# Optimization experiments

Hardware: AMD Instinct MI355X
Metric: run time of the kernel (lower is better)

Reference implementation:

```python
import jax, jax.numpy as jnp
import numpy as np

B, T, HOR, N = 32, 12, 12, 883
D = 10      # embed_dim == time_dim
HID = 64    # rnn_units
OUT = 1     # output_dim
K = 2       # cheb_k: supports [I, A]


def _pdg2(x, e1, e2, E, Wp, bp):
    # x:[B,N,Ci]  e1,e2:[B,N,D]  E:[N,D]  Wp:[D,K,Ci,Co]  bp:[D,Co]
    nv1 = jnp.tanh(E[None] * e1)                      # [B,N,D]
    nv2 = jnp.tanh(E[None] * e2)
    A = jax.nn.softmax(jax.nn.relu(jnp.einsum('bnd,bmd->bnm', nv1, nv2)), axis=-1)
    xg = jnp.stack([x, jnp.einsum('bnm,bmc->bnc', A, x)], axis=2)   # [B,N,K,Ci]
    W = jnp.einsum('bnd,dkio->bnkio', nv1, Wp)        # node/time-adaptive weights
    b = jnp.einsum('bnd,do->bno', nv1, bp)
    return jnp.einsum('bnki,bnkio->bno', xg, W) + b


def _cell(x, h, e1, e2, E, gW, gb, uW, ub):
    xs = jnp.concatenate([x, h], axis=-1)
    zr = jax.nn.sigmoid(_pdg2(xs, e1, e2, E, gW, gb))
    z, r = jnp.split(zr, 2, axis=-1)
    cand = jnp.concatenate([x, z * h], axis=-1)
    hc = jnp.tanh(_pdg2(cand, e1, e2, E, uW, ub))
    return r * h + (1.0 - r) * hc


def setup_inputs() -> dict:
    key = jax.random.key(0)
    ks = jax.random.split(key, 20)
    s = 0.1
    inp = {
        'src_vals': jax.random.normal(ks[0], (B, T, N, 1), jnp.float32),
        'node_emb': s * jax.random.normal(ks[1], (N, D), jnp.float32),
        'tid_emb1': s * jax.random.normal(ks[2], (288, D), jnp.float32),
        'tid_emb2': s * jax.random.normal(ks[3], (288, D), jnp.float32),
        'diw_emb1': s * jax.random.normal(ks[4], (7, D), jnp.float32),
        'diw_emb2': s * jax.random.normal(ks[5], (7, D), jnp.float32),
        'enc_gate_W': s * jax.random.normal(ks[6], (D, K, 1 + HID, 2 * HID), jnp.float32),
        'enc_gate_b': s * jax.random.normal(ks[7], (D, 2 * HID), jnp.float32),
        'enc_upd_W': s * jax.random.normal(ks[8], (D, K, 1 + HID, HID), jnp.float32),
        'enc_upd_b': s * jax.random.normal(ks[9], (D, HID), jnp.float32),
        'dec_gate_W': s * jax.random.normal(ks[10], (D, K, OUT + HID, 2 * HID), jnp.float32),
        'dec_gate_b': s * jax.random.normal(ks[11], (D, 2 * HID), jnp.float32),
        'dec_upd_W': s * jax.random.normal(ks[12], (D, K, OUT + HID, HID), jnp.float32),
        'dec_upd_b': s * jax.random.normal(ks[13], (D, HID), jnp.float32),
        'proj_W': s * jax.random.normal(ks[14], (OUT, HID), jnp.float32),
        'proj_b': jnp.zeros((OUT,), jnp.float32),
        'src_tid': jax.random.randint(ks[15], (B, T, N), 0, 288, jnp.int32),
        'src_diw': jax.random.randint(ks[16], (B, T, N), 0, 7, jnp.int32),
        'tgt_tid': jax.random.randint(ks[17], (B, HOR, N), 0, 288, jnp.int32),
        'tgt_diw': jax.random.randint(ks[18], (B, HOR, N), 0, 7, jnp.int32),
    }
    return inp


def reference(src_vals, node_emb, tid_emb1, tid_emb2, diw_emb1, diw_emb2,
              enc_gate_W, enc_gate_b, enc_upd_W, enc_upd_b,
              dec_gate_W, dec_gate_b, dec_upd_W, dec_upd_b,
              proj_W, proj_b, src_tid, src_diw, tgt_tid, tgt_diw):
    tm = lambda a: jnp.swapaxes(a, 0, 1)   # batch-major -> time-major
    # periodic embeddings (use_week=True -> elementwise product)
    e1_en = tid_emb1[src_tid] * diw_emb1[src_diw]   # [B,T,N,D]
    e2_en = tid_emb2[src_tid] * diw_emb2[src_diw]
    e1_de = tid_emb1[tgt_tid] * diw_emb1[tgt_diw]   # [B,HOR,N,D]
    e2_de = tid_emb2[tgt_tid] * diw_emb2[tgt_diw]

    h0 = jnp.zeros((src_vals.shape[0], node_emb.shape[0], HID), src_vals.dtype)

    def enc_step(h, inp):
        x, e1, e2 = inp
        h = _cell(x, h, e1, e2, node_emb, enc_gate_W, enc_gate_b, enc_upd_W, enc_upd_b)
        return h, None

    h, _ = jax.lax.scan(enc_step, h0, (tm(src_vals), tm(e1_en), tm(e2_en)))

    go0 = jnp.zeros((src_vals.shape[0], node_emb.shape[0], OUT), src_vals.dtype)

    def dec_step(carry, inp):
        h, go = carry
        e1, e2 = inp
        h = _cell(go, h, e1, e2, node_emb, dec_gate_W, dec_gate_b, dec_upd_W, dec_upd_b)
        go = h @ proj_W.T + proj_b
        return (h, go), go

    _, outs = jax.lax.scan(dec_step, (h, go0), (tm(e1_de), tm(e2_de)))
    return jnp.swapaxes(outs, 0, 1)   # [B,HOR,N,OUT]
```

## Files before the change

kernel.cpp:

```cpp
#include <hip/hip_runtime.h>

#define BB 32
#define TSRC 12
#define HORZ 12
#define NN 883
#define DD 10
#define HH 64
#define BN (BB*NN)
#define BNP 28288
#define KF 5
#define NT 14

typedef __attribute__((ext_vector_type(8))) short short8;
typedef __attribute__((ext_vector_type(4))) float f32x4;

static __device__ __forceinline__ float sigmf(float x) { return 1.f/(1.f + __expf(-x)); }
static __device__ __forceinline__ float tanh_fast(float x) {
  float e = __expf(2.f*x);
  return (e - 1.f) / (e + 1.f);
}
static __device__ __forceinline__ unsigned int bf_hi(float f) {
  unsigned int u = __float_as_uint(f);
  return (u + 0x7fffu + ((u >> 16) & 1u)) >> 16;
}
static __device__ __forceinline__ float bf_f(unsigned int h) {
  return __uint_as_float(h << 16);
}
static __device__ __forceinline__ void lds_load16(const void* g, void* l) {
  __builtin_amdgcn_global_load_lds(
      (const __attribute__((address_space(1))) void*)g,
      (__attribute__((address_space(3))) void*)l, 16, 0, 0);
}

static __device__ __forceinline__ void xs_store(unsigned short* chunk, int c, int mm2, float v) {
  int p0 = (c*128 + (mm2 ^ ((c & 7) << 4))) >> 1;
  unsigned int hi = bf_hi(v);
  chunk[p0] = (unsigned short)hi;
  chunk[p0 + 4096] = (unsigned short)bf_hi(v - bf_f(hi));
}

__global__ __launch_bounds__(256) void prep_kernel(
    const float* __restrict__ tidE1, const float* __restrict__ tidE2,
    const float* __restrict__ diwE1, const float* __restrict__ diwE2,
    const float* __restrict__ nodeE,
    const int* __restrict__ tididx, const int* __restrict__ diwidx,
    const float* __restrict__ xsrc, int xmode, int t, int tlen,
    float* __restrict__ nv1T, float* __restrict__ nv2T,
    unsigned short* __restrict__ XsH, unsigned short* __restrict__ XsZ)
{
  int i = blockIdx.x*256 + threadIdx.x;
  if (i >= BN) return;
  int b = i / NN, n = i - b*NN;
  int gi = (b*tlen + t)*NN + n;
  int ti = tididx[gi]*DD, di = diwidx[gi]*DD;
  int nE = n*DD;
#pragma unroll
  for (int d = 0; d < DD; ++d) {
    float E = nodeE[nE+d];
    nv1T[d*BNP+i] = tanh_fast(E * (tidE1[ti+d] * diwE1[di+d]));
    nv2T[d*BNP+i] = tanh_fast(E * (tidE2[ti+d] * diwE2[di+d]));
  }
  float xv = (xmode == 0) ? xsrc[gi] : xsrc[i];
  size_t cb = ((size_t)(b*NT + (n >> 6)))*8192;
  int mm = n & 63;
  unsigned int hi = bf_hi(xv);
  unsigned short los = (unsigned short)bf_hi(xv - bf_f(hi));
  XsH[cb + mm] = (unsigned short)hi; XsH[cb + 4096 + mm] = los;
  XsZ[cb + mm] = (unsigned short)hi; XsZ[cb + 4096 + mm] = los;
}

__global__ __launch_bounds__(256) void wsplit_kernel(
    const float* __restrict__ W, const float* __restrict__ bias,
    int NO, unsigned short* __restrict__ Wf)
{
  int i = blockIdx.x*256 + threadIdx.x;
  int total = DD*2*KF*4*NO*8;
  if (i >= total) return;
  int j = i & 7; int r = i >> 3;
  int o = r % NO; r /= NO;
  int quad = r & 3; r >>= 2;
  int kf = r % KF; r /= KF;
  int hl = r & 1; int d = r >> 1;
  int kk = kf*32 + quad*8 + j;
  float v = 0.f;
  if (kk <= 64)       v = W[(size_t)(d*130 + kk)*NO + o];
  else if (kk == 65)  v = bias[d*NO + o];
  else if (kk <= 130) v = W[(size_t)(d*130 + kk - 1)*NO + o];
  unsigned int hi = bf_hi(v);
  Wf[i] = (hl == 0) ? (unsigned short)hi : (unsigned short)bf_hi(v - bf_f(hi));
}

__global__ __launch_bounds__(256,3) void attn_kernel(
    const float* __restrict__ nv1T, const float* __restrict__ nv2T,
    const unsigned short* __restrict__ Xs,
    const float* __restrict__ hsrc,
    float* __restrict__ axT)
{
  __shared__ float nv1s[DD][64];
  __shared__ float nv2s[2][DD][64];
  __shared__ float xcolb[2][64];
  __shared__ alignas(16) unsigned short XT[8192];
  __shared__ alignas(16) unsigned short PT[2][64][72];
  __shared__ float linv[64];
  int b = blockIdx.y;
  int r0 = blockIdx.x*64;
  int tid = threadIdx.x;
  int rg = tid >> 4, cg = tid & 15;
  int base = b*NN;
  int lane = tid & 63, lm = lane & 15, quad = lane >> 4;
  int w = tid >> 6, mp = w >> 1, np = w & 1;
  const unsigned short* XsB = Xs + (size_t)b*NT*8192;

  for (int idx = tid; idx < DD*64; idx += 256) {
    int d = idx >> 6, r = idx & 63;
    nv1s[d][r] = (r0 + r < NN) ? nv1T[d*BNP + base + r0 + r] : 0.f;
  }

  int4 xt[4];
  float nvr[3]; float xcr;
  {
    const int4* s0 = (const int4*)XsB;
#pragma unroll
    for (int i = 0; i < 4; ++i) xt[i] = s0[w*64 + lane + i*256];
#pragma unroll
    for (int i = 0; i < 3; ++i) {
      int idx = tid + i*256; float v = 0.f;
      if (idx < DD*64) { int d = idx>>6, m = idx&63; v = (m < NN) ? nv2T[d*BNP + base + m] : 0.f; }
      nvr[i] = v;
    }
    xcr = (tid < 64 && tid < NN) ? hsrc[(size_t)63*BNP + base + tid] : 0.f;
#pragma unroll
    for (int i = 0; i < 4; ++i)
      *(int4*)((char*)XT + w*1024 + lane*16 + i*4096) = xt[i];
#pragma unroll
    for (int i = 0; i < 3; ++i) {
      int idx = tid + i*256;
      if (idx < DD*64) (&nv2s[0][0][0])[idx] = nvr[i];
    }
    if (tid < 64) xcolb[0][tid] = xcr;
  }
  __syncthreads();

  f32x4 accv[2][2] = {};
  float acclp[4] = {}, acc5p[4] = {};

  for (int tI = 0; tI < NT; ++tI) {
    int cur = tI & 1, nxt = cur ^ 1;
    int m0 = tI*64, m0n = m0 + 64;
    bool hasn = tI < NT-1;
    if (hasn) {
      const int4* src = (const int4*)(XsB + (size_t)(tI+1)*8192);
#pragma unroll
      for (int i = 0; i < 4; ++i) xt[i] = src[w*64 + lane + i*256];
#pragma unroll
      for (int i = 0; i < 3; ++i) {
        int idx = tid + i*256; float v = 0.f;
        if (idx < DD*64) { int d = idx>>6, m = idx&63; v = (m0n + m < NN) ? nv2T[d*BNP + base + m0n + m] : 0.f; }
        nvr[i] = v;
      }
      xcr = (tid < 64 && m0n + tid < NN) ? hsrc[(size_t)63*BNP + base + m0n + tid] : 0.f;
    }
    float s[4][4] = {};
#pragma unroll
    for (int d = 0; d < DD; ++d) {
      float4 a4 = *(const float4*)&nv1s[d][rg*4];
      float4 c4 = *(const float4*)&nv2s[cur][d][cg*4];
      const float* ap = (const float*)&a4;
      const float* cp = (const float*)&c4;
#pragma unroll
      for (int j = 0; j < 4; ++j)
#pragma unroll
        for (int jj = 0; jj < 4; ++jj)
          s[j][jj] += ap[j]*cp[jj];
    }
    int mvlim = NN - m0;
    float ev[4][4];
#pragma unroll
    for (int jj = 0; jj < 4; ++jj) {
      int m = cg*4 + jj;
      float xm = xcolb[cur][m];
      bool okm = m < mvlim;
#pragma unroll
      for (int j = 0; j < 4; ++j) {
        float e = okm ? __expf(fmaxf(s[j][jj], 0.f)) : 0.f;
        ev[j][jj] = e;
        acclp[j] += e;
        acc5p[j] = fmaf(e, xm, acc5p[j]);
      }
    }
    {
      unsigned int* P1 = (unsigned int*)&PT[0][0][0];
      unsigned int* P2 = (unsigned int*)&PT[1][0][0];
#pragma unroll
      for (int j = 0; j < 4; ++j) {
        int r = rg*4 + j;
        unsigned int h0 = bf_hi(ev[j][0]), h1 = bf_hi(ev[j][1]), h2 = bf_hi(ev[j][2]), h3 = bf_hi(ev[j][3]);
        unsigned int l0 = bf_hi(ev[j][0]-bf_f(h0)), l1 = bf_hi(ev[j][1]-bf_f(h1));
        unsigned int l2 = bf_hi(ev[j][2]-bf_f(h2)), l3 = bf_hi(ev[j][3]-bf_f(h3));
        int dw = r*36 + cg*2;
        P1[dw] = h0 | (h1 << 16); P1[dw+1] = h2 | (h3 << 16);
        P2[dw] = l0 | (l1 << 16); P2[dw+1] = l2 | (l3 << 16);
      }
    }
    __syncthreads();
    {
      short8 Aa[2][2], Ab[2][2], Ba[2][2], Bb[2][2];
#pragma unroll
      for (int mt = 0; mt < 2; ++mt) {
        int r = mp*32 + mt*16 + lm;
#pragma unroll
        for (int kf = 0; kf < 2; ++kf) {
          Aa[mt][kf] = *(const short8*)&PT[0][r][quad*8 + kf*32];
          Ab[mt][kf] = *(const short8*)&PT[1][r][quad*8 + kf*32];
        }
      }
#pragma unroll
      for (int ntl = 0; ntl < 2; ++ntl) {
        int c = np*32 + ntl*16 + lm;
        int swz = (c & 7) << 4;
        int cb0 = c*128 + quad*16;
#pragma unroll
        for (int kf = 0; kf < 2; ++kf) {
          int a = (cb0 + kf*64) ^ swz;
          Ba[ntl][kf] = *(const short8*)((const char*)XT + a);
          Bb[ntl][kf] = *(const short8*)((const char*)XT + a + 8192);
        }
      }
#pragma unroll
      for (int kf = 0; kf < 2; ++kf)
#pragma unroll
        for (int mt = 0; mt < 2; ++mt)
#pragma unroll
          for (int ntl = 0; ntl < 2; ++ntl) {
            accv[mt][ntl] = __builtin_amdgcn_mfma_f32_16x16x32_bf16(Aa[mt][kf], Ba[ntl][kf], accv[mt][ntl], 0,0,0);
            accv[mt][ntl] = __builtin_amdgcn_mfma_f32_16x16x32_bf16(Aa[mt][kf], Bb[ntl][kf], accv[mt][ntl], 0,0,0);
            accv[mt][ntl] = __builtin_amdgcn_mfma_f32_16x16x32_bf16(Ab[mt][kf], Ba[ntl][kf], accv[mt][ntl], 0,0,0);
          }
    }
    if (hasn) {
#pragma unroll
      for (int i = 0; i < 3; ++i) {
        int idx = tid + i*256;
        if (idx < DD*64) (&nv2s[nxt][0][0])[idx] = nvr[i];
      }
      if (tid < 64) xcolb[nxt][tid] = xcr;
    }
    __syncthreads();
    if (hasn) {
#pragma unroll
      for (int i = 0; i < 4; ++i)
        *(int4*)((char*)XT + w*1024 + lane*16 + i*4096) = xt[i];
    }
  }
#pragma unroll
  for (int off = 1; off <= 8; off <<= 1)
#pragma unroll
    for (int j = 0; j < 4; ++j) {
      acclp[j] += __shfl_xor(acclp[j], off, 64);
      acc5p[j] += __shfl_xor(acc5p[j], off, 64);
    }
  __syncthreads();
  if (cg == 0) {
#pragma unroll
    for (int j = 0; j < 4; ++j) {
      float li = 1.f / acclp[j];
      linv[rg*4 + j] = li;
      int r = r0 + rg*4 + j;
      if (r < NN) axT[(size_t)64*BNP + base + r] = acc5p[j]*li;
    }
  }
  __syncthreads();
  float* CT = (float*)&PT[0][0][0];
#pragma unroll
  for (int mt = 0; mt < 2; ++mt) {
    float4 lv = *(const float4*)&linv[mp*32 + mt*16 + quad*4];
    const float* lvp = (const float*)&lv;
#pragma unroll
    for (int ntl = 0; ntl < 2; ++ntl) {
      int c = np*32 + ntl*16 + lm;
#pragma unroll
      for (int r4 = 0; r4 < 4; ++r4)
        CT[(mp*32 + mt*16 + quad*4 + r4)*69 + c] = accv[mt][ntl][r4]*lvp[r4];
    }
  }
  __syncthreads();
  {
    int r = tid & 63, cb = tid >> 6;
    bool ok = (r0 + r) < NN;
    int gr = base + r0 + r;
#pragma unroll 4
    for (int i = 0; i < 16; ++i) {
      int c = cb*16 + i;
      if (ok) axT[(size_t)c*BNP + gr] = CT[r*69 + c];
    }
  }
}


__global__ __launch_bounds__(256,3) void gate_mfma(
    const float* __restrict__ xsrc, int xmode, int t, int tlen,
    const float* __restrict__ h,
    const float* __restrict__ axT,
    const float* __restrict__ nv1T,
    const unsigned short* __restrict__ Wf,
    float* __restrict__ zh, float* __restrict__ rbuf,
    unsigned short* __restrict__ XsZ)
{
  __shared__ alignas(16) unsigned char smem[46080];
  __shared__ float nvs[DD][64];
  unsigned short* XA = (unsigned short*)smem;
  unsigned int*  X1 = (unsigned int*)smem;
  int n0 = blockIdx.x*64, co0 = blockIdx.y*64;
  int tid = threadIdx.x;
  {
    int m = tid >> 2, ksub = tid & 3;
    int gm = n0 + m;
    float xv;
    if (xmode == 0) { int b = gm/NN; int n = gm - b*NN; xv = (gm < BN) ? xsrc[(b*tlen+t)*NN + n] : 0.f; }
    else xv = xsrc[gm];
#pragma unroll 4
    for (int i = 0; i < 20; ++i) {
      int kk = ksub*2 + 8*i;
      float v0, v1;
      if (kk == 0)        v0 = xv;
      else if (kk <= 64)  v0 = h[(size_t)(kk-1)*BNP + gm];
      else if (kk == 65)  v0 = 1.f;
      else if (kk <= 130) v0 = axT[(size_t)(kk-66)*BNP + gm];
      else v0 = 0.f;
      int k1 = kk + 1;
      if (k1 <= 64)       v1 = h[(size_t)(k1-1)*BNP + gm];
      else if (k1 == 65)  v1 = 1.f;
      else if (k1 <= 130) v1 = axT[(size_t)(k1-66)*BNP + gm];
      else v1 = 0.f;
      unsigned int h0 = bf_hi(v0), h1 = bf_hi(v1);
      unsigned int l0 = bf_hi(v0 - bf_f(h0)), l1 = bf_hi(v1 - bf_f(h1));
      int kf = kk >> 5, kkl = kk & 31;
      int dw = (kf*64 + m)*36 + (kkl >> 1);
      X1[dw] = h0 | (h1 << 16);
      X1[dw + 16] = l0 | (l1 << 16);
    }
  }
  for (int idx = tid; idx < DD*64; idx += 256)
    nvs[idx>>6][idx&63] = nv1T[(size_t)(idx>>6)*BNP + n0 + (idx&63)];
  __syncthreads();
  int w = tid >> 6, lane = tid & 63;
  int lm = lane & 15, quad = lane >> 4;
  int mp = w >> 1, np = w & 1;
  short8 A1[2][KF], A2[2][KF];
#pragma unroll
  for (int mt = 0; mt < 2; ++mt) {
    int mrow = mp*32 + mt*16 + lm;
#pragma unroll
    for (int kf = 0; kf < KF; ++kf) {
      A1[mt][kf] = *(const short8*)&XA[(kf*64 + mrow)*72 + quad*8];
      A2[mt][kf] = *(const short8*)&XA[(kf*64 + mrow)*72 + 32 + quad*8];
    }
  }
  __syncthreads();
  unsigned char* bufA = smem;
  unsigned char* bufB = smem + 20480;
  const int colb = np*32 + lm;
  {
    const unsigned short* src = Wf + ((size_t)(w*5)*128 + co0)*8 + lane*8;
#pragma unroll
    for (int i = 0; i < 5; ++i)
      lds_load16(src + (size_t)i*128*8, bufA + (w*5+i)*1024);
  }
  f32x4 accO[2][2] = {};
#pragma unroll 1
  for (int d = 0; d < DD; ++d) {
    f32x4 td[2][2] = {};
    __syncthreads();
    {
      const unsigned short* src = Wf + ((size_t)((d*2+1)*20 + w*5)*128 + co0)*8 + lane*8;
#pragma unroll
      for (int i = 0; i < 5; ++i)
        lds_load16(src + (size_t)i*128*8, bufB + (w*5+i)*1024);
    }
#pragma unroll
    for (int kf = 0; kf < KF; ++kf) {
      int cb = ((kf*4 + quad)*64 + colb)*16;
#pragma unroll
      for (int ntl = 0; ntl < 2; ++ntl) {
        short8 Bh = *(const short8*)(bufA + cb + ntl*256);
        td[0][ntl] = __builtin_amdgcn_mfma_f32_16x16x32_bf16(A1[0][kf], Bh, td[0][ntl], 0,0,0);
        td[0][ntl] = __builtin_amdgcn_mfma_f32_16x16x32_bf16(A2[0][kf], Bh, td[0][ntl], 0,0,0);
        td[1][ntl] = __builtin_amdgcn_mfma_f32_16x16x32_bf16(A1[1][kf], Bh, td[1][ntl], 0,0,0);
        td[1][ntl] = __builtin_amdgcn_mfma_f32_16x16x32_bf16(A2[1][kf], Bh, td[1][ntl], 0,0,0);
      }
    }
    __syncthreads();
    if (d < DD-1) {
      const unsigned short* src = Wf + ((size_t)((d+1)*2*20 + w*5)*128 + co0)*8 + lane*8;
#pragma unroll
      for (int i = 0; i < 5; ++i)
        lds_load16(src + (size_t)i*128*8, bufA + (w*5+i)*1024);
    }
#pragma unroll
    for (int kf = 0; kf < KF; ++kf) {
      int cb = ((kf*4 + quad)*64 + colb)*16;
#pragma unroll
      for (int ntl = 0; ntl < 2; ++ntl) {
        short8 Bl = *(const short8*)(bufB + cb + ntl*256);
        td[0][ntl] = __builtin_amdgcn_mfma_f32_16x16x32_bf16(A1[0][kf], Bl, td[0][ntl], 0,0,0);
        td[1][ntl] = __builtin_amdgcn_mfma_f32_16x16x32_bf16(A1[1][kf], Bl, td[1][ntl], 0,0,0);
      }
    }
#pragma unroll
    for (int mt = 0; mt < 2; ++mt) {
      float4 nv4 = *(const float4*)&nvs[d][mp*32 + mt*16 + quad*4];
      const float* nvp = (const float*)&nv4;
#pragma unroll
      for (int ntl = 0; ntl < 2; ++ntl)
#pragma unroll
        for (int r = 0; r < 4; ++r)
          accO[mt][ntl][r] += nvp[r] * td[mt][ntl][r];
    }
  }
  float* CT = (float*)smem;
  __syncthreads();
#pragma unroll
  for (int mt = 0; mt < 2; ++mt)
#pragma unroll
    for (int ntl = 0; ntl < 2; ++ntl)
#pragma unroll
      for (int r = 0; r < 4; ++r)
        CT[(mp*32 + mt*16 + quad*4 + r)*67 + np*32 + ntl*16 + lm] = accO[mt][ntl][r];
  __syncthreads();
  {
    int mm = tid & 63, og = tid >> 6;
    int gm = n0 + mm;
    if (co0 == 0) {
      bool okg = gm < BN;
      int bb = okg ? (gm / NN) : 0;
      int ml = gm - bb*NN;
      unsigned short* chk = XsZ + ((size_t)(bb*NT + (ml >> 6)))*8192;
      int mm2 = (ml & 63)*2;
      for (int j = 0; j < 16; ++j) {
        int o = og*16 + j;
        float z = sigmf(CT[mm*67 + o]);
        float zhv = z * h[(size_t)o*BNP + gm];
        zh[(size_t)o*BNP + gm] = zhv;
        if (okg && o < 63) xs_store(chk, o + 1, mm2, zhv);
      }
    } else {
      for (int j = 0; j < 16; ++j) {
        int o = og*16 + j;
        rbuf[(size_t)o*BNP + gm] = sigmf(CT[mm*67 + o]);
      }
    }
  }
}

__global__ __launch_bounds__(256,3) void upd_mfma(
    const float* __restrict__ xsrc, int xmode, int t, int tlen,
    const float* __restrict__ zh,
    const float* __restrict__ axT,
    const float* __restrict__ nv1T,
    const unsigned short* __restrict__ Wf,
    const float* __restrict__ rbuf, float* __restrict__ h,
    int dec, const float* __restrict__ pW, const float* __restrict__ pb,
    float* __restrict__ go, float* __restrict__ dout,
    unsigned short* __restrict__ XsH)
{
  __shared__ alignas(16) unsigned char smem[46080];
  __shared__ float nvs[DD][64];
  unsigned short* XA = (unsigned short*)smem;
  unsigned int*  X1 = (unsigned int*)smem;
  int n0 = blockIdx.x*64;
  int tid = threadIdx.x;
  {
    int m = tid >> 2, ksub = tid & 3;
    int gm = n0 + m;
    float xv;
    if (xmode == 0) { int b = gm/NN; int n = gm - b*NN; xv = (gm < BN) ? xsrc[(b*tlen+t)*NN + n] : 0.f; }
    else xv = xsrc[gm];
#pragma unroll 4
    for (int i = 0; i < 20; ++i) {
      int kk = ksub*2 + 8*i;
      float v0, v1;
      if (kk == 0)        v0 = xv;
      else if (kk <= 64)  v0 = zh[(size_t)(kk-1)*BNP + gm];
      else if (kk == 65)  v0 = 1.f;
      else if (kk <= 130) v0 = axT[(size_t)(kk-66)*BNP + gm];
      else v0 = 0.f;
      int k1 = kk + 1;
      if (k1 <= 64)       v1 = zh[(size_t)(k1-1)*BNP + gm];
      else if (k1 == 65)  v1 = 1.f;
      else if (k1 <= 130) v1 = axT[(size_t)(k1-66)*BNP + gm];
      else v1 = 0.f;
      unsigned int h0 = bf_hi(v0), h1 = bf_hi(v1);
      unsigned int l0 = bf_hi(v0 - bf_f(h0)), l1 = bf_hi(v1 - bf_f(h1));
      int kf = kk >> 5, kkl = kk & 31;
      int dw = (kf*64 + m)*36 + (kkl >> 1);
      X1[dw] = h0 | (h1 << 16);
      X1[dw + 16] = l0 | (l1 << 16);
    }
  }
  for (int idx = tid; idx < DD*64; idx += 256)
    nvs[idx>>6][idx&63] = nv1T[(size_t)(idx>>6)*BNP + n0 + (idx&63)];
  __syncthreads();
  int w = tid >> 6, lane = tid & 63;
  int lm = lane & 15, quad = lane >> 4;
  int mp = w >> 1, np = w & 1;
  short8 A1[2][KF], A2[2][KF];
#pragma unroll
  for (int mt = 0; mt < 2; ++mt) {
    int mrow = mp*32 + mt*16 + lm;
#pragma unroll
    for (int kf = 0; kf < KF; ++kf) {
      A1[mt][kf] = *(const short8*)&XA[(kf*64 + mrow)*72 + quad*8];
      A2[mt][kf] = *(const short8*)&XA[(kf*64 + mrow)*72 + 32 + quad*8];
    }
  }
  __syncthreads();
  unsigned char* bufA = smem;
  unsigned char* bufB = smem + 20480;
  const int colb = np*32 + lm;
  {
    const unsigned short* src = Wf + (size_t)(w*5)*64*8 + lane*8;
#pragma unroll
    for (int i = 0; i < 5; ++i)
      lds_load16(src + (size_t)i*64*8, bufA + (w*5+i)*1024);
  }
  f32x4 accO[2][2] = {};
#pragma unroll 1
  for (int d = 0; d < DD; ++d) {
    f32x4 td[2][2] = {};
    __syncthreads();
    {
      const unsigned short* src = Wf + (size_t)((d*2+1)*20 + w*5)*64*8 + lane*8;
#pragma unroll
      for (int i = 0; i < 5; ++i)
        lds_load16(src + (size_t)i*64*8, bufB + (w*5+i)*1024);
    }
#pragma unroll
    for (int kf = 0; kf < KF; ++kf) {
      int cb = ((kf*4 + quad)*64 + colb)*16;
#pragma unroll
      for (int ntl = 0; ntl < 2; ++ntl) {
        short8 Bh = *(const short8*)(bufA + cb + ntl*256);
        td[0][ntl] = __builtin_amdgcn_mfma_f32_16x16x32_bf16(A1[0][kf], Bh, td[0][ntl], 0,0,0);
        td[0][ntl] = __builtin_amdgcn_mfma_f32_16x16x32_bf16(A2[0][kf], Bh, td[0][ntl], 0,0,0);
        td[1][ntl] = __builtin_amdgcn_mfma_f32_16x16x32_bf16(A1[1][kf], Bh, td[1][ntl], 0,0,0);
        td[1][ntl] = __builtin_amdgcn_mfma_f32_16x16x32_bf16(A2[1][kf], Bh, td[1][ntl], 0,0,0);
      }
    }
    __syncthreads();
    if (d < DD-1) {
      const unsigned short* src = Wf + (size_t)((d+1)*2*20 + w*5)*64*8 + lane*8;
#pragma unroll
      for (int i = 0; i < 5; ++i)
        lds_load16(src + (size_t)i*64*8, bufA + (w*5+i)*1024);
    }
#pragma unroll
    for (int kf = 0; kf < KF; ++kf) {
      int cb = ((kf*4 + quad)*64 + colb)*16;
#pragma unroll
      for (int ntl = 0; ntl < 2; ++ntl) {
        short8 Bl = *(const short8*)(bufB + cb + ntl*256);
        td[0][ntl] = __builtin_amdgcn_mfma_f32_16x16x32_bf16(A1[0][kf], Bl, td[0][ntl], 0,0,0);
        td[1][ntl] = __builtin_amdgcn_mfma_f32_16x16x32_bf16(A1[1][kf], Bl, td[1][ntl], 0,0,0);
      }
    }
#pragma unroll
    for (int mt = 0; mt < 2; ++mt) {
      float4 nv4 = *(const float4*)&nvs[d][mp*32 + mt*16 + quad*4];
      const float* nvp = (const float*)&nv4;
#pragma unroll
      for (int ntl = 0; ntl < 2; ++ntl)
#pragma unroll
        for (int r = 0; r < 4; ++r)
          accO[mt][ntl][r] += nvp[r] * td[mt][ntl][r];
    }
  }
  float* CT = (float*)smem;
  __syncthreads();
#pragma unroll
  for (int mt = 0; mt < 2; ++mt)
#pragma unroll
    for (int ntl = 0; ntl < 2; ++ntl)
#pragma unroll
      for (int r = 0; r < 4; ++r)
        CT[(mp*32 + mt*16 + quad*4 + r)*67 + np*32 + ntl*16 + lm] = accO[mt][ntl][r];
  __syncthreads();
  {
    int mm = tid & 63, og = tid >> 6;
    int gm = n0 + mm;
    bool okg = gm < BN;
    int bb = okg ? (gm / NN) : 0;
    int ml = gm - bb*NN;
    unsigned short* chk = XsH + ((size_t)(bb*NT + (ml >> 6)))*8192;
    int mm2 = (ml & 63)*2;
    float pp = 0.f;
    for (int j = 0; j < 16; ++j) {
      int o = og*16 + j;
      float hc = tanhf(CT[mm*67 + o]);
      float r = rbuf[(size_t)o*BNP + gm];
      float hv = h[(size_t)o*BNP + gm];
      float hn = r*hv + (1.f - r)*hc;
      h[(size_t)o*BNP + gm] = hn;
      if (okg && o < 63) xs_store(chk, o + 1, mm2, hn);
      if (dec) pp = fmaf(hn, pW[o], pp);
    }
    if (dec) {
      float* PS = CT + 64*67;
      __syncthreads();
      PS[mm*4 + og] = pp;
      __syncthreads();
      if (tid < 64 && gm < BN) {
        float s = pb[0] + PS[tid*4] + PS[tid*4+1] + PS[tid*4+2] + PS[tid*4+3];
        go[gm] = s;
        int b = gm/NN, n = gm - b*NN;
        dout[(b*HORZ + t)*NN + n] = s;
      }
    }
  }
}

extern "C" void kernel_launch(void* const* d_in, const int* in_sizes, int n_in,
                              void* d_out, int out_size, void* d_ws, size_t ws_size,
                              hipStream_t stream) {
  (void)in_sizes; (void)n_in; (void)out_size; (void)ws_size;
  const float* src_vals = (const float*)d_in[0];
  const float* node_emb = (const float*)d_in[1];
  const float* tid1 = (const float*)d_in[2];
  const float* tid2 = (const float*)d_in[3];
  const float* diw1 = (const float*)d_in[4];
  const float* diw2 = (const float*)d_in[5];
  const float* egW = (const float*)d_in[6];
  const float* egb = (const float*)d_in[7];
  const float* euW = (const float*)d_in[8];
  const float* eub = (const float*)d_in[9];
  const float* dgW = (const float*)d_in[10];
  const float* dgb = (const float*)d_in[11];
  const float* duW = (const float*)d_in[12];
  const float* dub = (const float*)d_in[13];
  const float* pW  = (const float*)d_in[14];
  const float* pb  = (const float*)d_in[15];
  const int* stid = (const int*)d_in[16];
  const int* sdiw = (const int*)d_in[17];
  const int* ttid = (const int*)d_in[18];
  const int* tdiw = (const int*)d_in[19];
  float* out = (float*)d_out;

  float* wp = (float*)d_ws;
  float* hbuf = wp; wp += (size_t)64*BNP;
  float* zh   = wp; wp += (size_t)64*BNP;
  float* rbuf = wp; wp += (size_t)64*BNP;
  float* axT  = wp; wp += (size_t)65*BNP;
  float* nv1T = wp; wp += (size_t)DD*BNP;
  float* nv2T = wp; wp += (size_t)DD*BNP;
  float* go   = wp; wp += BN + 64;
  unsigned short* egS = (unsigned short*)wp; wp += 204800;
  unsigned short* dgS = (unsigned short*)wp; wp += 204800;
  unsigned short* euS = (unsigned short*)wp; wp += 102400;
  unsigned short* duS = (unsigned short*)wp; wp += 102400;
  unsigned short* XsH = (unsigned short*)wp; wp += 1835008;
  unsigned short* XsZ = (unsigned short*)wp; wp += 1835008;

  hipMemsetAsync(hbuf, 0, sizeof(float)*(size_t)64*BNP, stream);
  hipMemsetAsync(go, 0, sizeof(float)*(BN+64), stream);
  hipMemsetAsync(XsH, 0, (size_t)BB*NT*16384, stream);
  hipMemsetAsync(XsZ, 0, (size_t)BB*NT*16384, stream);

  wsplit_kernel<<<1600,256,0,stream>>>(egW, egb, 128, egS);
  wsplit_kernel<<<1600,256,0,stream>>>(dgW, dgb, 128, dgS);
  wsplit_kernel<<<800,256,0,stream>>>(euW, eub, 64, euS);
  wsplit_kernel<<<800,256,0,stream>>>(duW, dub, 64, duS);

  dim3 agrid(NT, BB);
  dim3 ggrid(442, 2);
  for (int t = 0; t < TSRC; ++t) {
    prep_kernel<<<111,256,0,stream>>>(tid1,tid2,diw1,diw2,node_emb,stid,sdiw,src_vals,0,t,TSRC,nv1T,nv2T,XsH,XsZ);
    attn_kernel<<<agrid,256,0,stream>>>(nv1T,nv2T,XsH,hbuf,axT);
    gate_mfma<<<ggrid,256,0,stream>>>(src_vals,0,t,TSRC,hbuf,axT,nv1T,egS,zh,rbuf,XsZ);
    attn_kernel<<<agrid,256,0,stream>>>(nv1T,nv2T,XsZ,zh,axT);
    upd_mfma<<<442,256,0,stream>>>(src_vals,0,t,TSRC,zh,axT,nv1T,euS,rbuf,hbuf,0,pW,pb,go,out,XsH);
  }
  for (int t = 0; t < HORZ; ++t) {
    prep_kernel<<<111,256,0,stream>>>(tid1,tid2,diw1,diw2,node_emb,ttid,tdiw,go,1,t,HORZ,nv1T,nv2T,XsH,XsZ);
    attn_kernel<<<agrid,256,0,stream>>>(nv1T,nv2T,XsH,hbuf,axT);
    gate_mfma<<<ggrid,256,0,stream>>>(go,1,t,HORZ,hbuf,axT,nv1T,dgS,zh,rbuf,XsZ);
    attn_kernel<<<agrid,256,0,stream>>>(nv1T,nv2T,XsZ,zh,axT);
    upd_mfma<<<442,256,0,stream>>>(go,1,t,HORZ,zh,axT,nv1T,duS,rbuf,hbuf,1,pW,pb,go,out,XsH);
  }
}
```

Baseline: 4.863 ms.

## Fuse graph attention with gate and update GEMMs into per-block kernels

Merges the attention kernel with the following gate and update MFMA kernels so that the aggregated A·x result is written straight into shared memory as bf16 hi/lo operands. It no longer goes through the global axT buffer. This removes the axT write and re-read and two launches per cell step. In exchange, each fused block now covers both gate output halves serially over a 14x32 grid rather than 442x2. That reduces parallelism and may leave the GPU underfilled during the GEMM phase.

```diff
diff --git a/kernel.cpp b/kernel.cpp
--- a/kernel.cpp
+++ b/kernel.cpp
@@ -90,20 +90,24 @@
   Wf[i] = (hl == 0) ? (unsigned short)hi : (unsigned short)bf_hi(v - bf_f(hi));
 }
 
-__global__ __launch_bounds__(256,3) void attn_kernel(
+
+__global__ __launch_bounds__(256,3) void attn_gate(
     const float* __restrict__ nv1T, const float* __restrict__ nv2T,
     const unsigned short* __restrict__ Xs,
     const float* __restrict__ hsrc,
-    float* __restrict__ axT)
+    const float* __restrict__ xsrc, int xmode, int t, int tlen,
+    const unsigned short* __restrict__ Wf,
+    float* __restrict__ zh, float* __restrict__ rbuf,
+    unsigned short* __restrict__ XsZ)
 {
   __shared__ float nv1s[DD][64];
-  __shared__ float nv2s[2][DD][64];
-  __shared__ float xcolb[2][64];
-  __shared__ alignas(16) unsigned short XT[8192];
-  __shared__ alignas(16) unsigned short PT[2][64][72];
   __shared__ float linv[64];
-  int b = blockIdx.y;
-  int r0 = blockIdx.x*64;
+  __shared__ alignas(16) unsigned char U[46080];
+  unsigned short* XT = (unsigned short*)U;
+  unsigned short* PT = (unsigned short*)(U + 16384);
+  float* nv2s = (float*)(U + 34816);
+  float* xcolb = (float*)(U + 39936);
+  int b = blockIdx.y, r0 = blockIdx.x*64;
   int tid = threadIdx.x;
   int rg = tid >> 4, cg = tid & 15;
   int base = b*NN;
@@ -135,9 +139,9 @@
 #pragma unroll
     for (int i = 0; i < 3; ++i) {
       int idx = tid + i*256;
-      if (idx < DD*64) (&nv2s[0][0][0])[idx] = nvr[i];
-    }
-    if (tid < 64) xcolb[0][tid] = xcr;
+      if (idx < DD*64) nv2s[idx] = nvr[i];
+    }
+    if (tid < 64) xcolb[tid] = xcr;
   }
   __syncthreads();
 
@@ -164,7 +168,7 @@
 #pragma unroll
     for (int d = 0; d < DD; ++d) {
       float4 a4 = *(const float4*)&nv1s[d][rg*4];
-      float4 c4 = *(const float4*)&nv2s[cur][d][cg*4];
+      float4 c4 = *(const float4*)&nv2s[cur*(DD*64) + d*64 + cg*4];
       const float* ap = (const float*)&a4;
       const float* cp = (const float*)&c4;
 #pragma unroll
@@ -178,7 +182,7 @@
 #pragma unroll
     for (int jj = 0; jj < 4; ++jj) {
       int m = cg*4 + jj;
-      float xm = xcolb[cur][m];
+      float xm = xcolb[cur*64 + m];
       bool okm = m < mvlim;
 #pragma unroll
       for (int j = 0; j < 4; ++j) {
@@ -189,8 +193,8 @@
       }
     }
     {
-      unsigned int* P1 = (unsigned int*)&PT[0][0][0];
-      unsigned int* P2 = (unsigned int*)&PT[1][0][0];
+      unsigned int* P1 = (unsigned int*)PT;
+      unsigned int* P2 = (unsigned int*)(PT + 64*72);
 #pragma unroll
       for (int j = 0; j < 4; ++j) {
         int r = rg*4 + j;
@@ -210,8 +214,8 @@
         int r = mp*32 + mt*16 + lm;
 #pragma unroll
         for (int kf = 0; kf < 2; ++kf) {
-          Aa[mt][kf] = *(const short8*)&PT[0][r][quad*8 + kf*32];
-          Ab[mt][kf] = *(const short8*)&PT[1][r][quad*8 + kf*32];
+          Aa[mt][kf] = *(const short8*)&PT[r*72 + quad*8 + kf*32];
+          Ab[mt][kf] = *(const short8*)&PT[64*72 + r*72 + quad*8 + kf*32];
         }
       }
 #pragma unroll
@@ -241,15 +245,31 @@
 #pragma unroll
       for (int i = 0; i < 3; ++i) {
         int idx = tid + i*256;
-        if (idx < DD*64) (&nv2s[nxt][0][0])[idx] = nvr[i];
-      }
-      if (tid < 64) xcolb[nxt][tid] = xcr;
+        if (idx < DD*64) nv2s[nxt*(DD*64) + idx] = nvr[i];
+      }
+      if (tid < 64) xcolb[nxt*64 + tid] = xcr;
     }
     __syncthreads();
     if (hasn) {
 #pragma unroll
       for (int i = 0; i < 4; ++i)
         *(int4*)((char*)XT + w*1024 + lane*16 + i*4096) = xt[i];
+    }
+  }
+  int mrow_x = tid >> 2, ksub = tid & 3;
+  int gmx = base + r0 + mrow_x;
+  float hv0[9], hv1[9];
+  {
+    bool nok = (r0 + mrow_x) < NN;
+    float xv;
+    if (xmode == 0) xv = nok ? xsrc[(b*tlen+t)*NN + r0 + mrow_x] : 0.f;
+    else xv = xsrc[gmx];
+#pragma unroll
+    for (int i = 0; i < 9; ++i) {
+      int kk = ksub*2 + 8*i;
+      if (kk > 64) { hv0[i] = 0.f; hv1[i] = 0.f; continue; }
+      hv0[i] = (kk == 0) ? xv : hsrc[(size_t)(kk-1)*BNP + gmx];
+      hv1[i] = (kk == 64) ? 1.f : hsrc[(size_t)kk*BNP + gmx];
     }
   }
 #pragma unroll
@@ -260,92 +280,61 @@
       acc5p[j] += __shfl_xor(acc5p[j], off, 64);
     }
   __syncthreads();
+  {
+    unsigned int* Z = (unsigned int*)(U + 36864);
+    for (int idx = tid; idx < 2304; idx += 256) Z[idx] = 0;
+  }
+  __syncthreads();
+  unsigned short* XA = (unsigned short*)U;
   if (cg == 0) {
 #pragma unroll
     for (int j = 0; j < 4; ++j) {
       float li = 1.f / acclp[j];
-      linv[rg*4 + j] = li;
-      int r = r0 + rg*4 + j;
-      if (r < NN) axT[(size_t)64*BNP + base + r] = acc5p[j]*li;
-    }
-  }
-  __syncthreads();
-  float* CT = (float*)&PT[0][0][0];
+      int r = rg*4 + j;
+      linv[r] = li;
+      float v = acc5p[j]*li;
+      unsigned int hi = bf_hi(v);
+      XA[(4*64 + r)*72 + 2] = (unsigned short)hi;
+      XA[(4*64 + r)*72 + 32 + 2] = (unsigned short)bf_hi(v - bf_f(hi));
+    }
+  }
+  __syncthreads();
 #pragma unroll
   for (int mt = 0; mt < 2; ++mt) {
-    float4 lv = *(const float4*)&linv[mp*32 + mt*16 + quad*4];
+    int rbase = mp*32 + mt*16 + quad*4;
+    float4 lv = *(const float4*)&linv[rbase];
     const float* lvp = (const float*)&lv;
 #pragma unroll
     for (int ntl = 0; ntl < 2; ++ntl) {
       int c = np*32 + ntl*16 + lm;
-#pragma unroll
-      for (int r4 = 0; r4 < 4; ++r4)
-        CT[(mp*32 + mt*16 + quad*4 + r4)*69 + c] = accv[mt][ntl][r4]*lvp[r4];
-    }
-  }
-  __syncthreads();
-  {
-    int r = tid & 63, cb = tid >> 6;
-    bool ok = (r0 + r) < NN;
-    int gr = base + r0 + r;
-#pragma unroll 4
-    for (int i = 0; i < 16; ++i) {
-      int c = cb*16 + i;
-      if (ok) axT[(size_t)c*BNP + gr] = CT[r*69 + c];
-    }
-  }
-}
-
-
-__global__ __launch_bounds__(256,3) void gate_mfma(
-    const float* __restrict__ xsrc, int xmode, int t, int tlen,
-    const float* __restrict__ h,
-    const float* __restrict__ axT,
-    const float* __restrict__ nv1T,
-    const unsigned short* __restrict__ Wf,
-    float* __restrict__ zh, float* __restrict__ rbuf,
-    unsigned short* __restrict__ XsZ)
-{
-  __shared__ alignas(16) unsigned char smem[46080];
-  __shared__ float nvs[DD][64];
-  unsigned short* XA = (unsigned short*)smem;
-  unsigned int*  X1 = (unsigned int*)smem;
-  int n0 = blockIdx.x*64, co0 = blockIdx.y*64;
-  int tid = threadIdx.x;
-  {
-    int m = tid >> 2, ksub = tid & 3;
-    int gm = n0 + m;
-    float xv;
-    if (xmode == 0) { int b = gm/NN; int n = gm - b*NN; xv = (gm < BN) ? xsrc[(b*tlen+t)*NN + n] : 0.f; }
-    else xv = xsrc[gm];
-#pragma unroll 4
-    for (int i = 0; i < 20; ++i) {
+      int kk = 66 + c;
+      int kf = kk >> 5, kkl = kk & 31;
+#pragma unroll
+      for (int r4 = 0; r4 < 4; ++r4) {
+        float v = accv[mt][ntl][r4] * lvp[r4];
+        unsigned int hi = bf_hi(v);
+        int p = (kf*64 + rbase + r4)*72 + kkl;
+        XA[p] = (unsigned short)hi;
+        XA[p + 32] = (unsigned short)bf_hi(v - bf_f(hi));
+      }
+    }
+  }
+  {
+    unsigned int* X1 = (unsigned int*)U;
+#pragma unroll
+    for (int i = 0; i < 9; ++i) {
       int kk = ksub*2 + 8*i;
-      float v0, v1;
-      if (kk == 0)        v0 = xv;
-      else if (kk <= 64)  v0 = h[(size_t)(kk-1)*BNP + gm];
-      else if (kk == 65)  v0 = 1.f;
-      else if (kk <= 130) v0 = axT[(size_t)(kk-66)*BNP + gm];
-      else v0 = 0.f;
-      int k1 = kk + 1;
-      if (k1 <= 64)       v1 = h[(size_t)(k1-1)*BNP + gm];
-      else if (k1 == 65)  v1 = 1.f;
-      else if (k1 <= 130) v1 = axT[(size_t)(k1-66)*BNP + gm];
-      else v1 = 0.f;
+      if (kk > 64) continue;
+      float v0 = hv0[i], v1 = hv1[i];
       unsigned int h0 = bf_hi(v0), h1 = bf_hi(v1);
       unsigned int l0 = bf_hi(v0 - bf_f(h0)), l1 = bf_hi(v1 - bf_f(h1));
       int kf = kk >> 5, kkl = kk & 31;
-      int dw = (kf*64 + m)*36 + (kkl >> 1);
+      int dw = (kf*64 + mrow_x)*36 + (kkl >> 1);
       X1[dw] = h0 | (h1 << 16);
       X1[dw + 16] = l0 | (l1 << 16);
     }
   }
-  for (int idx = tid; idx < DD*64; idx += 256)
-    nvs[idx>>6][idx&63] = nv1T[(size_t)(idx>>6)*BNP + n0 + (idx&63)];
-  __syncthreads();
-  int w = tid >> 6, lane = tid & 63;
-  int lm = lane & 15, quad = lane >> 4;
-  int mp = w >> 1, np = w & 1;
+  __syncthreads();
   short8 A1[2][KF], A2[2][KF];
 #pragma unroll
   for (int mt = 0; mt < 2; ++mt) {
@@ -357,152 +346,354 @@
     }
   }
   __syncthreads();
-  unsigned char* bufA = smem;
-  unsigned char* bufB = smem + 20480;
+  unsigned char* bufA = U;
+  unsigned char* bufB = U + 20480;
   const int colb = np*32 + lm;
-  {
-    const unsigned short* src = Wf + ((size_t)(w*5)*128 + co0)*8 + lane*8;
-#pragma unroll
-    for (int i = 0; i < 5; ++i)
-      lds_load16(src + (size_t)i*128*8, bufA + (w*5+i)*1024);
-  }
-  f32x4 accO[2][2] = {};
 #pragma unroll 1
-  for (int d = 0; d < DD; ++d) {
-    f32x4 td[2][2] = {};
+  for (int co = 0; co < 2; ++co) {
+    int co0 = co*64;
+    {
+      const unsigned short* src = Wf + ((size_t)(w*5)*128 + co0)*8 + lane*8;
+#pragma unroll
+      for (int i = 0; i < 5; ++i)
+        lds_load16(src + (size_t)i*128*8, bufA + (w*5+i)*1024);
+    }
+    f32x4 accO[2][2] = {};
+#pragma unroll 1
+    for (int d = 0; d < DD; ++d) {
+      f32x4 td[2][2] = {};
+      __syncthreads();
+      {
+        const unsigned short* src = Wf + ((size_t)((d*2+1)*20 + w*5)*128 + co0)*8 + lane*8;
+#pragma unroll
+        for (int i = 0; i < 5; ++i)
+          lds_load16(src + (size_t)i*128*8, bufB + (w*5+i)*1024);
+      }
+#pragma unroll
+      for (int kf = 0; kf < KF; ++kf) {
+        int cb = ((kf*4 + quad)*64 + colb)*16;
+#pragma unroll
+        for (int ntl = 0; ntl < 2; ++ntl) {
+          short8 Bh = *(const short8*)(bufA + cb + ntl*256);
+          td[0][ntl] = __builtin_amdgcn_mfma_f32_16x16x32_bf16(A1[0][kf], Bh, td[0][ntl], 0,0,0);
+          td[0][ntl] = __builtin_amdgcn_mfma_f32_16x16x32_bf16(A2[0][kf], Bh, td[0][ntl], 0,0,0);
+          td[1][ntl] = __builtin_amdgcn_mfma_f32_16x16x32_bf16(A1[1][kf], Bh, td[1][ntl], 0,0,0);
+          td[1][ntl] = __builtin_amdgcn_mfma_f32_16x16x32_bf16(A2[1][kf], Bh, td[1][ntl], 0,0,0);
+        }
+      }
+      __syncthreads();
+      if (d < DD-1) {
+        const unsigned short* src = Wf + ((size_t)((d+1)*2*20 + w*5)*128 + co0)*8 + lane*8;
+#pragma unroll
+        for (int i = 0; i < 5; ++i)
+          lds_load16(src + (size_t)i*128*8, bufA + (w*5+i)*1024);
+      }
+#pragma unroll
+      for (int kf = 0; kf < KF; ++kf) {
+        int cb = ((kf*4 + quad)*64 + colb)*16;
+#pragma unroll
+        for (int ntl = 0; ntl < 2; ++ntl) {
+          short8 Bl = *(const short8*)(bufB + cb + ntl*256);
+          td[0][ntl] = __builtin_amdgcn_mfma_f32_16x16x32_bf16(A1[0][kf], Bl, td[0][ntl], 0,0,0);
+          td[1][ntl] = __builtin_amdgcn_mfma_f32_16x16x32_bf16(A1[1][kf], Bl, td[1][ntl], 0,0,0);
+        }
+      }
+#pragma unroll
+      for (int mt = 0; mt < 2; ++mt) {
+        float4 nv4 = *(const float4*)&nv1s[d][mp*32 + mt*16 + quad*4];
+        const float* nvp = (const float*)&nv4;
+#pragma unroll
+        for (int ntl = 0; ntl < 2; ++ntl)
+#pragma unroll
+          for (int r = 0; r < 4; ++r)
+            accO[mt][ntl][r] += nvp[r] * td[mt][ntl][r];
+      }
+    }
+    float* CT = (float*)U;
+    __syncthreads();
+#pragma unroll
+    for (int mt = 0; mt < 2; ++mt)
+#pragma unroll
+      for (int ntl = 0; ntl < 2; ++ntl)
+#pragma unroll
+        for (int r = 0; r < 4; ++r)
+          CT[(mp*32 + mt*16 + quad*4 + r)*67 + np*32 + ntl*16 + lm] = accO[mt][ntl][r];
     __syncthreads();
     {
-      const unsigned short* src = Wf + ((size_t)((d*2+1)*20 + w*5)*128 + co0)*8 + lane*8;
-#pragma unroll
-      for (int i = 0; i < 5; ++i)
-        lds_load16(src + (size_t)i*128*8, bufB + (w*5+i)*1024);
-    }
-#pragma unroll
-    for (int kf = 0; kf < KF; ++kf) {
-      int cb = ((kf*4 + quad)*64 + colb)*16;
-#pragma unroll
-      for (int ntl = 0; ntl < 2; ++ntl) {
-        short8 Bh = *(const short8*)(bufA + cb + ntl*256);
-        td[0][ntl] = __builtin_amdgcn_mfma_f32_16x16x32_bf16(A1[0][kf], Bh, td[0][ntl], 0,0,0);
-        td[0][ntl] = __builtin_amdgcn_mfma_f32_16x16x32_bf16(A2[0][kf], Bh, td[0][ntl], 0,0,0);
-        td[1][ntl] = __builtin_amdgcn_mfma_f32_16x16x32_bf16(A1[1][kf], Bh, td[1][ntl], 0,0,0);
-        td[1][ntl] = __builtin_amdgcn_mfma_f32_16x16x32_bf16(A2[1][kf], Bh, td[1][ntl], 0,0,0);
+      int mm = tid & 63, og = tid >> 6;
+      int n = r0 + mm;
+      int gm = base + n;
+      bool okn = n < NN;
+      if (co == 0) {
+        unsigned short* chk = XsZ + ((size_t)(b*NT + blockIdx.x))*8192;
+        int mm2 = mm*2;
+        for (int j = 0; j < 16; ++j) {
+          int o = og*16 + j;
+          float z = sigmf(CT[mm*67 + o]);
+          float zhv = z * hsrc[(size_t)o*BNP + gm];
+          if (okn) {
+            zh[(size_t)o*BNP + gm] = zhv;
+            if (o < 63) xs_store(chk, o + 1, mm2, zhv);
+          }
+        }
+      } else {
+        for (int j = 0; j < 16; ++j) {
+          int o = og*16 + j;
+          if (okn) rbuf[(size_t)o*BNP + gm] = sigmf(CT[mm*67 + o]);
+        }
       }
     }
     __syncthreads();
-    if (d < DD-1) {
-      const unsigned short* src = Wf + ((size_t)((d+1)*2*20 + w*5)*128 + co0)*8 + lane*8;
-#pragma unroll
-      for (int i = 0; i < 5; ++i)
-        lds_load16(src + (size_t)i*128*8, bufA + (w*5+i)*1024);
-    }
-#pragma unroll
-    for (int kf = 0; kf < KF; ++kf) {
-      int cb = ((kf*4 + quad)*64 + colb)*16;
-#pragma unroll
-      for (int ntl = 0; ntl < 2; ++ntl) {
-        short8 Bl = *(const short8*)(bufB + cb + ntl*256);
-        td[0][ntl] = __builtin_amdgcn_mfma_f32_16x16x32_bf16(A1[0][kf], Bl, td[0][ntl], 0,0,0);
-        td[1][ntl] = __builtin_amdgcn_mfma_f32_16x16x32_bf16(A1[1][kf], Bl, td[1][ntl], 0,0,0);
-      }
-    }
-#pragma unroll
-    for (int mt = 0; mt < 2; ++mt) {
-      float4 nv4 = *(const float4*)&nvs[d][mp*32 + mt*16 + quad*4];
-      const float* nvp = (const float*)&nv4;
-#pragma unroll
-      for (int ntl = 0; ntl < 2; ++ntl)
-#pragma unroll
-        for (int r = 0; r < 4; ++r)
-          accO[mt][ntl][r] += nvp[r] * td[mt][ntl][r];
-    }
-  }
-  float* CT = (float*)smem;
-  __syncthreads();
-#pragma unroll
-  for (int mt = 0; mt < 2; ++mt)
-#pragma unroll
-    for (int ntl = 0; ntl < 2; ++ntl)
-#pragma unroll
-      for (int r = 0; r < 4; ++r)
-        CT[(mp*32 + mt*16 + quad*4 + r)*67 + np*32 + ntl*16 + lm] = accO[mt][ntl][r];
-  __syncthreads();
-  {
-    int mm = tid & 63, og = tid >> 6;
-    int gm = n0 + mm;
-    if (co0 == 0) {
-      bool okg = gm < BN;
-      int bb = okg ? (gm / NN) : 0;
-      int ml = gm - bb*NN;
-      unsigned short* chk = XsZ + ((size_t)(bb*NT + (ml >> 6)))*8192;
-      int mm2 = (ml & 63)*2;
-      for (int j = 0; j < 16; ++j) {
-        int o = og*16 + j;
-        float z = sigmf(CT[mm*67 + o]);
-        float zhv = z * h[(size_t)o*BNP + gm];
-        zh[(size_t)o*BNP + gm] = zhv;
-        if (okg && o < 63) xs_store(chk, o + 1, mm2, zhv);
-      }
-    } else {
-      for (int j = 0; j < 16; ++j) {
-        int o = og*16 + j;
-        rbuf[(size_t)o*BNP + gm] = sigmf(CT[mm*67 + o]);
-      }
-    }
-  }
-}
-
-__global__ __launch_bounds__(256,3) void upd_mfma(
+  }
+}
+
+__global__ __launch_bounds__(256,3) void attn_upd(
+    const float* __restrict__ nv1T, const float* __restrict__ nv2T,
+    const unsigned short* __restrict__ Xs,
+    const float* __restrict__ hsrc,
+    const float* __restrict__ hstate,
     const float* __restrict__ xsrc, int xmode, int t, int tlen,
-    const float* __restrict__ zh,
-    const float* __restrict__ axT,
-    const float* __restrict__ nv1T,
     const unsigned short* __restrict__ Wf,
-    const float* __restrict__ rbuf, float* __restrict__ h,
+    const float* __restrict__ rbuf,
     int dec, const float* __restrict__ pW, const float* __restrict__ pb,
     float* __restrict__ go, float* __restrict__ dout,
     unsigned short* __restrict__ XsH)
 {
-  __shared__ alignas(16) unsigned char smem[46080];
-  __shared__ float nvs[DD][64];
-  unsigned short* XA = (unsigned short*)smem;
-  unsigned int*  X1 = (unsigned int*)smem;
-  int n0 = blockIdx.x*64;
+  __shared__ float nv1s[DD][64];
+  __shared__ float linv[64];
+  __shared__ alignas(16) unsigned char U[46080];
+  unsigned short* XT = (unsigned short*)U;
+  unsigned short* PT = (unsigned short*)(U + 16384);
+  float* nv2s = (float*)(U + 34816);
+  float* xcolb = (float*)(U + 39936);
+  int b = blockIdx.y, r0 = blockIdx.x*64;
   int tid = threadIdx.x;
-  {
-    int m = tid >> 2, ksub = tid & 3;
-    int gm = n0 + m;
+  int rg = tid >> 4, cg = tid & 15;
+  int base = b*NN;
+  int lane = tid & 63, lm = lane & 15, quad = lane >> 4;
+  int w = tid >> 6, mp = w >> 1, np = w & 1;
+  const unsigned short* XsB = Xs + (size_t)b*NT*8192;
+
+  for (int idx = tid; idx < DD*64; idx += 256) {
+    int d = idx >> 6, r = idx & 63;
+    nv1s[d][r] = (r0 + r < NN) ? nv1T[d*BNP + base + r0 + r] : 0.f;
+  }
+
+  int4 xt[4];
+  float nvr[3]; float xcr;
+  {
+    const int4* s0 = (const int4*)XsB;
+#pragma unroll
+    for (int i = 0; i < 4; ++i) xt[i] = s0[w*64 + lane + i*256];
+#pragma unroll
+    for (int i = 0; i < 3; ++i) {
+      int idx = tid + i*256; float v = 0.f;
+      if (idx < DD*64) { int d = idx>>6, m = idx&63; v = (m < NN) ? nv2T[d*BNP + base + m] : 0.f; }
+      nvr[i] = v;
+    }
+    xcr = (tid < 64 && tid < NN) ? hsrc[(size_t)63*BNP + base + tid] : 0.f;
+#pragma unroll
+    for (int i = 0; i < 4; ++i)
+      *(int4*)((char*)XT + w*1024 + lane*16 + i*4096) = xt[i];
+#pragma unroll
+    for (int i = 0; i < 3; ++i) {
+      int idx = tid + i*256;
+      if (idx < DD*64) nv2s[idx] = nvr[i];
+    }
+    if (tid < 64) xcolb[tid] = xcr;
+  }
+  __syncthreads();
+
+  f32x4 accv[2][2] = {};
+  float acclp[4] = {}, acc5p[4] = {};
+
+  for (int tI = 0; tI < NT; ++tI) {
+    int cur = tI & 1, nxt = cur ^ 1;
+    int m0 = tI*64, m0n = m0 + 64;
+    bool hasn = tI < NT-1;
+    if (hasn) {
+      const int4* src = (const int4*)(XsB + (size_t)(tI+1)*8192);
+#pragma unroll
+      for (int i = 0; i < 4; ++i) xt[i] = src[w*64 + lane + i*256];
+#pragma unroll
+      for (int i = 0; i < 3; ++i) {
+        int idx = tid + i*256; float v = 0.f;
+        if (idx < DD*64) { int d = idx>>6, m = idx&63; v = (m0n + m < NN) ? nv2T[d*BNP + base + m0n + m] : 0.f; }
+        nvr[i] = v;
+      }
+      xcr = (tid < 64 && m0n + tid < NN) ? hsrc[(size_t)63*BNP + base + m0n + tid] : 0.f;
+    }
+    float s[4][4] = {};
+#pragma unroll
+    for (int d = 0; d < DD; ++d) {
+      float4 a4 = *(const float4*)&nv1s[d][rg*4];
+      float4 c4 = *(const float4*)&nv2s[cur*(DD*64) + d*64 + cg*4];
+      const float* ap = (const float*)&a4;
+      const float* cp = (const float*)&c4;
+#pragma unroll
+      for (int j = 0; j < 4; ++j)
+#pragma unroll
+        for (int jj = 0; jj < 4; ++jj)
+          s[j][jj] += ap[j]*cp[jj];
+    }
+    int mvlim = NN - m0;
+    float ev[4][4];
+#pragma unroll
+    for (int jj = 0; jj < 4; ++jj) {
+      int m = cg*4 + jj;
+      float xm = xcolb[cur*64 + m];
+      bool okm = m < mvlim;
+#pragma unroll
+      for (int j = 0; j < 4; ++j) {
+        float e = okm ? __expf(fmaxf(s[j][jj], 0.f)) : 0.f;
+        ev[j][jj] = e;
+        acclp[j] += e;
+        acc5p[j] = fmaf(e, xm, acc5p[j]);
+      }
+    }
+    {
+      unsigned int* P1 = (unsigned int*)PT;
+      unsigned int* P2 = (unsigned int*)(PT + 64*72);
+#pragma unroll
+      for (int j = 0; j < 4; ++j) {
+        int r = rg*4 + j;
+        unsigned int h0 = bf_hi(ev[j][0]), h1 = bf_hi(ev[j][1]), h2 = bf_hi(ev[j][2]), h3 = bf_hi(ev[j][3]);
+        unsigned int l0 = bf_hi(ev[j][0]-bf_f(h0)), l1 = bf_hi(ev[j][1]-bf_f(h1));
+        unsigned int l2 = bf_hi(ev[j][2]-bf_f(h2)), l3 = bf_hi(ev[j][3]-bf_f(h3));
+        int dw = r*36 + cg*2;
+        P1[dw] = h0 | (h1 << 16); P1[dw+1] = h2 | (h3 << 16);
+        P2[dw] = l0 | (l1 << 16); P2[dw+1] = l2 | (l3 << 16);
+      }
+    }
+    __syncthreads();
+    {
+      short8 Aa[2][2], Ab[2][2], Ba[2][2], Bb[2][2];
+#pragma unroll
+      for (int mt = 0; mt < 2; ++mt) {
+        int r = mp*32 + mt*16 + lm;
+#pragma unroll
+        for (int kf = 0; kf < 2; ++kf) {
+          Aa[mt][kf] = *(const short8*)&PT[r*72 + quad*8 + kf*32];
+          Ab[mt][kf] = *(const short8*)&PT[64*72 + r*72 + quad*8 + kf*32];
+        }
+      }
+#pragma unroll
+      for (int ntl = 0; ntl < 2; ++ntl) {
+        int c = np*32 + ntl*16 + lm;
+        int swz = (c & 7) << 4;
+        int cb0 = c*128 + quad*16;
+#pragma unroll
+        for (int kf = 0; kf < 2; ++kf) {
+          int a = (cb0 + kf*64) ^ swz;
+          Ba[ntl][kf] = *(const short8*)((const char*)XT + a);
+          Bb[ntl][kf] = *(const short8*)((const char*)XT + a + 8192);
+        }
+      }
+#pragma unroll
+      for (int kf = 0; kf < 2; ++kf)
+#pragma unroll
+        for (int mt = 0; mt < 2; ++mt)
+#pragma unroll
+          for (int ntl = 0; ntl < 2; ++ntl) {
+            accv[mt][ntl] = __builtin_amdgcn_mfma_f32_16x16x32_bf16(Aa[mt][kf], Ba[ntl][kf], accv[mt][ntl], 0,0,0);
+            accv[mt][ntl] = __builtin_amdgcn_mfma_f32_16x16x32_bf16(Aa[mt][kf], Bb[ntl][kf], accv[mt][ntl], 0,0,0);
+            accv[mt][ntl] = __builtin_amdgcn_mfma_f32_16x16x32_bf16(Ab[mt][kf], Ba[ntl][kf], accv[mt][ntl], 0,0,0);
+          }
+    }
+    if (hasn) {
+#pragma unroll
+      for (int i = 0; i < 3; ++i) {
+        int idx = tid + i*256;
+        if (idx < DD*64) nv2s[nxt*(DD*64) + idx] = nvr[i];
+      }
+      if (tid < 64) xcolb[nxt*64 + tid] = xcr;
+    }
+    __syncthreads();
+    if (hasn) {
+#pragma unroll
+      for (int i = 0; i < 4; ++i)
+        *(int4*)((char*)XT + w*1024 + lane*16 + i*4096) = xt[i];
+    }
+  }
+  int mrow_x = tid >> 2, ksub = tid & 3;
+  int gmx = base + r0 + mrow_x;
+  float hv0[9], hv1[9];
+  {
+    bool nok = (r0 + mrow_x) < NN;
     float xv;
-    if (xmode == 0) { int b = gm/NN; int n = gm - b*NN; xv = (gm < BN) ? xsrc[(b*tlen+t)*NN + n] : 0.f; }
-    else xv = xsrc[gm];
-#pragma unroll 4
-    for (int i = 0; i < 20; ++i) {
+    if (xmode == 0) xv = nok ? xsrc[(b*tlen+t)*NN + r0 + mrow_x] : 0.f;
+    else xv = xsrc[gmx];
+#pragma unroll
+    for (int i = 0; i < 9; ++i) {
       int kk = ksub*2 + 8*i;
-      float v0, v1;
-      if (kk == 0)        v0 = xv;
-      else if (kk <= 64)  v0 = zh[(size_t)(kk-1)*BNP + gm];
-      else if (kk == 65)  v0 = 1.f;
-      else if (kk <= 130) v0 = axT[(size_t)(kk-66)*BNP + gm];
-      else v0 = 0.f;
-      int k1 = kk + 1;
-      if (k1 <= 64)       v1 = zh[(size_t)(k1-1)*BNP + gm];
-      else if (k1 == 65)  v1 = 1.f;
-      else if (k1 <= 130) v1 = axT[(size_t)(k1-66)*BNP + gm];
-      else v1 = 0.f;
+      if (kk > 64) { hv0[i] = 0.f; hv1[i] = 0.f; continue; }
+      hv0[i] = (kk == 0) ? xv : hsrc[(size_t)(kk-1)*BNP + gmx];
+      hv1[i] = (kk == 64) ? 1.f : hsrc[(size_t)kk*BNP + gmx];
+    }
+  }
+#pragma unroll
+  for (int off = 1; off <= 8; off <<= 1)
+#pragma unroll
+    for (int j = 0; j < 4; ++j) {
+      acclp[j] += __shfl_xor(acclp[j], off, 64);
+      acc5p[j] += __shfl_xor(acc5p[j], off, 64);
+    }
+  __syncthreads();
+  {
+    unsigned int* Z = (unsigned int*)(U + 36864);
+    for (int idx = tid; idx < 2304; idx += 256) Z[idx] = 0;
+  }
+  __syncthreads();
+  unsigned short* XA = (unsigned short*)U;
+  if (cg == 0) {
+#pragma unroll
+    for (int j = 0; j < 4; ++j) {
+      float li = 1.f / acclp[j];
+      int r = rg*4 + j;
+      linv[r] = li;
+      float v = acc5p[j]*li;
+      unsigned int hi = bf_hi(v);
+      XA[(4*64 + r)*72 + 2] = (unsigned short)hi;
+      XA[(4*64 + r)*72 + 32 + 2] = (unsigned short)bf_hi(v - bf_f(hi));
+    }
+  }
+  __syncthreads();
+#pragma unroll
+  for (int mt = 0; mt < 2; ++mt) {
+    int rbase = mp*32 + mt*16 + quad*4;
+    float4 lv = *(const float4*)&linv[rbase];
+    const float* lvp = (const float*)&lv;
+#pragma unroll
+    for (int ntl = 0; ntl < 2; ++ntl) {
+      int c = np*32 + ntl*16 + lm;
+      int kk = 66 + c;
+      int kf = kk >> 5, kkl = kk & 31;
+#pragma unroll
+      for (int r4 = 0; r4 < 4; ++r4) {
+        float v = accv[mt][ntl][r4] * lvp[r4];
+        unsigned int hi = bf_hi(v);
+        int p = (kf*64 + rbase + r4)*72 + kkl;
+        XA[p] = (unsigned short)hi;
+        XA[p + 32] = (unsigned short)bf_hi(v - bf_f(hi));
+      }
+    }
+  }
+  {
+    unsigned int* X1 = (unsigned int*)U;
+#pragma unroll
+    for (int i = 0; i < 9; ++i) {
+      int kk = ksub*2 + 8*i;
+      if (kk > 64) continue;
+      float v0 = hv0[i], v1 = hv1[i];
       unsigned int h0 = bf_hi(v0), h1 = bf_hi(v1);
       unsigned int l0 = bf_hi(v0 - bf_f(h0)), l1 = bf_hi(v1 - bf_f(h1));
       int kf = kk >> 5, kkl = kk & 31;
-      int dw = (kf*64 + m)*36 + (kkl >> 1);
+      int dw = (kf*64 + mrow_x)*36 + (kkl >> 1);
       X1[dw] = h0 | (h1 << 16);
       X1[dw + 16] = l0 | (l1 << 16);
     }
   }
-  for (int idx = tid; idx < DD*64; idx += 256)
-    nvs[idx>>6][idx&63] = nv1T[(size_t)(idx>>6)*BNP + n0 + (idx&63)];
-  __syncthreads();
-  int w = tid >> 6, lane = tid & 63;
-  int lm = lane & 15, quad = lane >> 4;
-  int mp = w >> 1, np = w & 1;
+  __syncthreads();
   short8 A1[2][KF], A2[2][KF];
 #pragma unroll
   for (int mt = 0; mt < 2; ++mt) {
@@ -514,8 +705,8 @@
     }
   }
   __syncthreads();
-  unsigned char* bufA = smem;
-  unsigned char* bufB = smem + 20480;
+  unsigned char* bufA = U;
+  unsigned char* bufB = U + 20480;
   const int colb = np*32 + lm;
   {
     const unsigned short* src = Wf + (size_t)(w*5)*64*8 + lane*8;
@@ -565,7 +756,7 @@
     }
 #pragma unroll
     for (int mt = 0; mt < 2; ++mt) {
-      float4 nv4 = *(const float4*)&nvs[d][mp*32 + mt*16 + quad*4];
+      float4 nv4 = *(const float4*)&nv1s[d][mp*32 + mt*16 + quad*4];
       const float* nvp = (const float*)&nv4;
 #pragma unroll
       for (int ntl = 0; ntl < 2; ++ntl)
@@ -574,7 +765,7 @@
           accO[mt][ntl][r] += nvp[r] * td[mt][ntl][r];
     }
   }
-  float* CT = (float*)smem;
+  float* CT = (float*)U;
   __syncthreads();
 #pragma unroll
   for (int mt = 0; mt < 2; ++mt)
@@ -586,21 +777,22 @@
   __syncthreads();
   {
     int mm = tid & 63, og = tid >> 6;
-    int gm = n0 + mm;
-    bool okg = gm < BN;
-    int bb = okg ? (gm / NN) : 0;
-    int ml = gm - bb*NN;
-    unsigned short* chk = XsH + ((size_t)(bb*NT + (ml >> 6)))*8192;
-    int mm2 = (ml & 63)*2;
+    int n = r0 + mm;
+    int gm = base + n;
+    bool okn = n < NN;
+    unsigned short* chk = XsH + ((size_t)(b*NT + blockIdx.x))*8192;
+    int mm2 = mm*2;
     float pp = 0.f;
     for (int j = 0; j < 16; ++j) {
       int o = og*16 + j;
       float hc = tanhf(CT[mm*67 + o]);
       float r = rbuf[(size_t)o*BNP + gm];
-      float hv = h[(size_t)o*BNP + gm];
+      float hv = hstate[(size_t)o*BNP + gm];
       float hn = r*hv + (1.f - r)*hc;
-      h[(size_t)o*BNP + gm] = hn;
-      if (okg && o < 63) xs_store(chk, o + 1, mm2, hn);
+      if (okn) {
+        ((float*)hstate)[(size_t)o*BNP + gm] = hn;
+        if (o < 63) xs_store(chk, o + 1, mm2, hn);
+      }
       if (dec) pp = fmaf(hn, pW[o], pp);
     }
     if (dec) {
@@ -608,11 +800,13 @@
       __syncthreads();
       PS[mm*4 + og] = pp;
       __syncthreads();
-      if (tid < 64 && gm < BN) {
-        float s = pb[0] + PS[tid*4] + PS[tid*4+1] + PS[tid*4+2] + PS[tid*4+3];
-        go[gm] = s;
-        int b = gm/NN, n = gm - b*NN;
-        dout[(b*HORZ + t)*NN + n] = s;
+      if (tid < 64) {
+        int n2 = r0 + tid;
+        if (n2 < NN) {
+          float s = pb[0] + PS[tid*4] + PS[tid*4+1] + PS[tid*4+2] + PS[tid*4+3];
+          go[base + n2] = s;
+          dout[(b*HORZ + t)*NN + n2] = s;
+        }
       }
     }
   }
@@ -648,7 +842,6 @@
   float* hbuf = wp; wp += (size_t)64*BNP;
   float* zh   = wp; wp += (size_t)64*BNP;
   float* rbuf = wp; wp += (size_t)64*BNP;
-  float* axT  = wp; wp += (size_t)65*BNP;
   float* nv1T = wp; wp += (size_t)DD*BNP;
   float* nv2T = wp; wp += (size_t)DD*BNP;
   float* go   = wp; wp += BN + 64;
@@ -669,20 +862,15 @@
   wsplit_kernel<<<800,256,0,stream>>>(euW, eub, 64, euS);
   wsplit_kernel<<<800,256,0,stream>>>(duW, dub, 64, duS);
 
-  dim3 agrid(NT, BB);
-  dim3 ggrid(442, 2);
+  dim3 fgrid(NT, BB);
   for (int t = 0; t < TSRC; ++t) {
     prep_kernel<<<111,256,0,stream>>>(tid1,tid2,diw1,diw2,node_emb,stid,sdiw,src_vals,0,t,TSRC,nv1T,nv2T,XsH,XsZ);
-    attn_kernel<<<agrid,256,0,stream>>>(nv1T,nv2T,XsH,hbuf,axT);
-    gate_mfma<<<ggrid,256,0,stream>>>(src_vals,0,t,TSRC,hbuf,axT,nv1T,egS,zh,rbuf,XsZ);
-    attn_kernel<<<agrid,256,0,stream>>>(nv1T,nv2T,XsZ,zh,axT);
-    upd_mfma<<<442,256,0,stream>>>(src_vals,0,t,TSRC,zh,axT,nv1T,euS,rbuf,hbuf,0,pW,pb,go,out,XsH);
+    attn_gate<<<fgrid,256,0,stream>>>(nv1T,nv2T,XsH,hbuf,src_vals,0,t,TSRC,egS,zh,rbuf,XsZ);
+    attn_upd<<<fgrid,256,0,stream>>>(nv1T,nv2T,XsZ,zh,hbuf,src_vals,0,t,TSRC,euS,rbuf,0,pW,pb,go,out,XsH);
   }
   for (int t = 0; t < HORZ; ++t) {
     prep_kernel<<<111,256,0,stream>>>(tid1,tid2,diw1,diw2,node_emb,ttid,tdiw,go,1,t,HORZ,nv1T,nv2T,XsH,XsZ);
-    attn_kernel<<<agrid,256,0,stream>>>(nv1T,nv2T,XsH,hbuf,axT);
-    gate_mfma<<<ggrid,256,0,stream>>>(go,1,t,HORZ,hbuf,axT,nv1T,dgS,zh,rbuf,XsZ);
-    attn_kernel<<<agrid,256,0,stream>>>(nv1T,nv2T,XsZ,zh,axT);
-    upd_mfma<<<442,256,0,stream>>>(go,1,t,HORZ,zh,axT,nv1T,duS,rbuf,hbuf,1,pW,pb,go,out,XsH);
-  }
-}
+    attn_gate<<<fgrid,256,0,stream>>>(nv1T,nv2T,XsH,hbuf,go,1,t,HORZ,dgS,zh,rbuf,XsZ);
+    attn_upd<<<fgrid,256,0,stream>>>(nv1T,nv2T,XsZ,zh,hbuf,go,1,t,HORZ,duS,rbuf,1,pW,pb,go,out,XsH);
+  }
+}
```

After: 4.658 ms. -4.2%, faster.
